# Optimization experiments

Hardware: AMD Instinct MI355X
Metric: run time of the kernel (lower is better)

The kernel has to match this reference:

```python
import jax, jax.numpy as jnp
from jax import lax
import numpy as np

A = 9                 # 3 scales x 3 ratios
PRE_NMS_TOPN = 4000
POST_NMS_TOPN = 2000
NMS_THRESH = 0.7
MIN_SIZE = 16.0       # min_size * im_scale (im_info scale = 1)
NEG_INF = -1e9


def generate_anchors(base_size=16, ratios=(0.5, 1.0, 2.0), scales=(8, 16, 32)):
    ratios = np.array(ratios, dtype=np.float64)
    scales = np.array(scales, dtype=np.float64)
    w = h = float(base_size)
    xc = yc = 0.5 * (base_size - 1)
    size = w * h
    ws_r = np.round(np.sqrt(size / ratios))          # [3]
    hs_r = np.round(ws_r * ratios)                   # [3]
    ws = (ws_r[:, None] * scales[None, :]).reshape(-1)   # [9]
    hs = (hs_r[:, None] * scales[None, :]).reshape(-1)   # [9]
    anchors = np.stack([xc - 0.5 * (ws - 1), yc - 0.5 * (hs - 1),
                        xc + 0.5 * (ws - 1), yc + 0.5 * (hs - 1)], axis=1)
    return anchors.astype(np.float32)                # [9,4]


def _conv(x, w, b, padding):
    y = lax.conv_general_dilated(x, w, (1, 1), padding,
                                 dimension_numbers=('NCHW', 'OIHW', 'NCHW'))
    return y + b[None, :, None, None]


def _bbox_transform_inv(anchors, deltas):
    w = anchors[:, 2] - anchors[:, 0] + 1.0
    h = anchors[:, 3] - anchors[:, 1] + 1.0
    cx = anchors[:, 0] + 0.5 * w
    cy = anchors[:, 1] + 0.5 * h
    pcx = deltas[:, 0] * w + cx
    pcy = deltas[:, 1] * h + cy
    pw = jnp.exp(deltas[:, 2]) * w
    ph = jnp.exp(deltas[:, 3]) * h
    return jnp.stack([pcx - 0.5 * pw, pcy - 0.5 * ph,
                      pcx + 0.5 * pw, pcy + 0.5 * ph], axis=1)


def _greedy_nms(boxes, keep_init, thresh):
    # boxes already sorted by descending score; keep_init masks invalid rows
    x1, y1, x2, y2 = boxes[:, 0], boxes[:, 1], boxes[:, 2], boxes[:, 3]
    areas = (x2 - x1 + 1.0) * (y2 - y1 + 1.0)
    xx1 = jnp.maximum(x1[:, None], x1[None, :])
    yy1 = jnp.maximum(y1[:, None], y1[None, :])
    xx2 = jnp.minimum(x2[:, None], x2[None, :])
    yy2 = jnp.minimum(y2[:, None], y2[None, :])
    inter = jnp.maximum(0.0, xx2 - xx1 + 1.0) * jnp.maximum(0.0, yy2 - yy1 + 1.0)
    iou = inter / (areas[:, None] + areas[None, :] - inter)   # [N,N]
    n = boxes.shape[0]
    idx = jnp.arange(n)

    def body(i, keep):
        suppress = keep[i] & (iou[i] > thresh) & (idx > i)
        return keep & ~suppress

    return lax.fori_loop(0, n, body, keep_init)


def reference(im, feats, w_conv, b_conv, w_cls, b_cls, w_reg, b_reg):
    im_h, im_w = im.shape[2], im.shape[3]
    fh, fw = feats.shape[2], feats.shape[3]
    stride = round(im_w / fw)

    # RPN head (classifier)
    hid = jax.nn.relu(_conv(feats, w_conv, b_conv, 'SAME'))
    rpn_map = _conv(hid, w_cls, b_cls, 'SAME')       # [1, 2A, fh, fw]
    rpn_bbox = _conv(hid, w_reg, b_reg, 'SAME')      # [1, 4A, fh, fw]

    # anchor generation: [K*A, 4], shift-major / anchor-minor
    base = jnp.asarray(generate_anchors())
    sx = jnp.arange(fw, dtype=jnp.float32) * stride
    sy = jnp.arange(fh, dtype=jnp.float32) * stride
    sxx, syy = jnp.meshgrid(sx, sy)                  # [fh, fw]
    shifts = jnp.stack([sxx.ravel(), syy.ravel(), sxx.ravel(), syy.ravel()], 1)
    anchors = (base[None, :, :] + shifts[:, None, :]).reshape(-1, 4)

    # predictions, flattened in (h, w, a) order to match anchors
    deltas = rpn_bbox.transpose(0, 2, 3, 1).reshape(-1, 4)
    scores = rpn_map[:, A:, :, :].transpose(0, 2, 3, 1).reshape(-1)

    proposals = _bbox_transform_inv(anchors, deltas)
    # clip_boxes to image
    proposals = jnp.stack([
        jnp.clip(proposals[:, 0], 0.0, im_w - 1.0),
        jnp.clip(proposals[:, 1], 0.0, im_h - 1.0),
        jnp.clip(proposals[:, 2], 0.0, im_w - 1.0),
        jnp.clip(proposals[:, 3], 0.0, im_h - 1.0)], axis=1)

    # filter_boxes (min_size) expressed as a score mask (jit-friendly)
    ws = proposals[:, 2] - proposals[:, 0] + 1.0
    hs = proposals[:, 3] - proposals[:, 1] + 1.0
    valid = (ws >= MIN_SIZE) & (hs >= MIN_SIZE)
    masked_scores = jnp.where(valid, scores, NEG_INF)

    # sort descending, take pre_nms_topN
    order = jnp.argsort(-masked_scores)[:PRE_NMS_TOPN]
    top_boxes = proposals[order]
    top_scores = masked_scores[order]
    keep_init = top_scores > NEG_INF / 2

    keep = _greedy_nms(top_boxes, keep_init, NMS_THRESH)

    # take first post_nms_topN kept (already in score order), padded with zeros
    rank = jnp.cumsum(keep) - 1
    take = keep & (rank < POST_NMS_TOPN)
    dst = jnp.where(take, rank, 0)
    out_boxes = jnp.zeros((POST_NMS_TOPN, 4), dtype=top_boxes.dtype)
    out_boxes = out_boxes.at[dst].add(jnp.where(take[:, None], top_boxes, 0.0))
    out_scores = jnp.zeros((POST_NMS_TOPN, 1), dtype=top_scores.dtype)
    out_scores = out_scores.at[dst].add(jnp.where(take[:, None], top_scores[:, None], 0.0))
    return out_boxes, out_scores


def setup_inputs() -> dict:
    key = jax.random.key(0)
    ks = jax.random.split(key, 8)
    # small weight scale keeps exp(dw) in a sane range, as a trained RPN would
    return {
        'im': jax.random.normal(ks[0], (1, 3, 800, 1216), jnp.float32),
        'feats': jax.random.normal(ks[1], (1, 1024, 50, 76), jnp.float32),
        'w_conv': jax.random.normal(ks[2], (512, 1024, 3, 3), jnp.float32) * 0.001,
        'b_conv': jnp.zeros((512,), jnp.float32),
        'w_cls': jax.random.normal(ks[3], (18, 512, 1, 1), jnp.float32) * 0.01,
        'b_cls': jnp.zeros((18,), jnp.float32),
        'w_reg': jax.random.normal(ks[4], (36, 512, 1, 1), jnp.float32) * 0.01,
        'b_reg': jnp.zeros((36,), jnp.float32),
    }
```

## Files before the change

kernel.cpp:

```cpp
#include <hip/hip_runtime.h>
#include <stdint.h>
#include <math.h>

typedef unsigned long long u64;
typedef unsigned int u32;

#define CIN     1024
#define COUT    512
#define FH      50
#define FW      76
#define QP      80
#define HIDP    4096
#define FPITCH  4160
#define NPOS    3800
#define NA      34200
#define PRE_N   4000
#define POST_N  2000
#define MASKW   63
#define TBN     4032
#define KSLICES 8
#define CPS     128
#define QT      256

#define P0 (3*CIN*FPITCH)
#define P2 (512*48)
#define P3 65536

__device__ __forceinline__ void async16(const float* g, float* l) {
  __builtin_amdgcn_global_load_lds(
      (__attribute__((address_space(1))) void*)(g),
      (__attribute__((address_space(3))) void*)(l), 16, 0, 0);
}

__global__ void k_prep(const float* __restrict__ feats,
                       const float* __restrict__ w_cls, const float* __restrict__ b_cls,
                       const float* __restrict__ w_reg, const float* __restrict__ b_reg,
                       float* __restrict__ fpad3, float* __restrict__ wT, float* __restrict__ bT,
                       u32* __restrict__ hist, u32* __restrict__ ctrl,
                       double4* __restrict__ tb, float* __restrict__ ts) {
  int idx = blockIdx.x * 256 + threadIdx.x;
  if (idx < P0) {
    int tc = idx / (CIN * FPITCH);
    int rem = idx - tc * (CIN * FPITCH);
    int cin = rem / FPITCH;
    int j = rem - cin * FPITCH + tc;
    float v = 0.f;
    if (j < FPITCH) {
      int r = j / QP, u = j - r * QP;
      if (r >= 1 && r <= FH && u >= 1 && u <= FW)
        v = feats[cin * (FH * FW) + (r - 1) * FW + (u - 1)];
    }
    fpad3[idx] = v;
    return;
  }
  idx -= P0;
  if (idx < P2) {
    int c = idx / 48, o = idx - c * 48;
    float v = 0.f;
    if (o < 9) v = w_cls[(size_t)(9 + o) * 512 + c];
    else if (o < 45) v = w_reg[(size_t)(o - 9) * 512 + c];
    wT[idx] = v;
    return;
  }
  idx -= P2;
  if (idx < P3) {
    hist[idx] = 0;
    if (idx < 8) ctrl[idx] = 0;
    if (idx < 48) bT[idx] = (idx < 9) ? b_cls[9 + idx] : (idx < 45 ? b_reg[idx - 9] : 0.f);
    if (idx >= PRE_N && idx < TBN) { tb[idx] = make_double4(0.0, 0.0, 0.0, 0.0); ts[idx] = -1.0e9f; }
  }
}

__global__ void k_wt(const float* __restrict__ w, float* __restrict__ wt) {
  __shared__ float t[64][65];
  int k0 = blockIdx.x * 64, oc0 = blockIdx.y * 64;
  int tx = threadIdx.x & 63, tg = threadIdx.x >> 6;
#pragma unroll
  for (int rr = 0; rr < 16; rr++) {
    int row = tg * 16 + rr;
    t[row][tx] = w[(size_t)(oc0 + row) * 9216 + k0 + tx];
  }
  __syncthreads();
#pragma unroll
  for (int rr = 0; rr < 16; rr++) {
    int kr = tg * 16 + rr;
    wt[(size_t)(k0 + kr) * 512 + oc0 + tx] = t[tx][kr];
  }
}

__global__ __launch_bounds__(256, 4) void k_conv(const float* __restrict__ fpad3,
                                                 const float* __restrict__ wt,
                                                 float* __restrict__ hidp) {
  __shared__ __align__(16) float Bl[3][9][QT];
  const int tid = threadIdx.x;
  const int lane = tid & 63;
  const int wv = __builtin_amdgcn_readfirstlane(tid >> 6);
  const int q0 = blockIdx.x * QT;
  const int ws = (blockIdx.y << 2) + wv;
  const int c0 = blockIdx.z * CPS;

  const int rA = wv;
  const int rB = wv + 4;
  u32 offA = (u32)(rA % 3) * (CIN * FPITCH) + (u32)(rA / 3) * QP + q0 + lane * 4;
  u32 offB = (u32)(rB % 3) * (CIN * FPITCH) + (u32)(rB / 3) * QP + q0 + lane * 4;
  u32 offC = 2u * (CIN * FPITCH) + 2u * QP + q0 + lane * 4;

  float acc32[8][4];
  double acc64[8][4];
#pragma unroll
  for (int i = 0; i < 8; i++)
#pragma unroll
    for (int j = 0; j < 4; j++) { acc32[i][j] = 0.f; acc64[i][j] = 0.0; }

#define STAGE(buf, s)  do {                                                     \
    const float* _b = fpad3 + (size_t)(c0 + (s)) * FPITCH;                      \
    async16(_b + offA, &Bl[buf][rA][0]);                                        \
    async16(_b + offB, &Bl[buf][rB][0]);                                        \
    if (wv == 0) async16(_b + offC, &Bl[buf][8][0]);                            \
  } while (0)

  STAGE(0, 0);
  STAGE(1, 1);

#pragma unroll 1
  for (int s = 0; s < CPS; s++) {
    if (s + 1 < CPS) {
      if (wv == 0) asm volatile("s_waitcnt vmcnt(3)" ::: "memory");
      else         asm volatile("s_waitcnt vmcnt(2)" ::: "memory");
    } else {
      asm volatile("s_waitcnt vmcnt(0)" ::: "memory");
    }
    __builtin_amdgcn_s_barrier();
    __builtin_amdgcn_sched_barrier(0);
    const int b0 = s % 3;
    if (s + 2 < CPS) STAGE((s + 2) % 3, s + 2);
    const float* wp = wt + ((size_t)(c0 + s) * 9 << 9) + (ws << 3);
#pragma unroll
    for (int ks = 0; ks < 9; ks++) {
      float4 b4 = *(const float4*)&Bl[b0][ks][lane * 4];
      const float* w8 = wp + (ks << 9);
#pragma unroll
      for (int i = 0; i < 8; i++) {
        float w = w8[i];
        acc32[i][0] = fmaf(w, b4.x, acc32[i][0]);
        acc32[i][1] = fmaf(w, b4.y, acc32[i][1]);
        acc32[i][2] = fmaf(w, b4.z, acc32[i][2]);
        acc32[i][3] = fmaf(w, b4.w, acc32[i][3]);
      }
    }
    if ((s & 7) == 7) {
#pragma unroll
      for (int i = 0; i < 8; i++)
#pragma unroll
        for (int j = 0; j < 4; j++) { acc64[i][j] += (double)acc32[i][j]; acc32[i][j] = 0.f; }
    }
  }
#undef STAGE

#pragma unroll
  for (int i = 0; i < 8; i++) {
    float4 o;
    o.x = (float)acc64[i][0];
    o.y = (float)acc64[i][1];
    o.z = (float)acc64[i][2];
    o.w = (float)acc64[i][3];
    *(float4*)&hidp[((size_t)(blockIdx.z * COUT + (ws << 3) + i) << 12) + q0 + lane * 4] = o;
  }
}

__global__ void k_reduce(const float* __restrict__ hidp, const float* __restrict__ bconv,
                         float* __restrict__ hid) {
  int idx = blockIdx.x * 256 + threadIdx.x;
  int oc = idx >> 12;
  double s = 0.0;
#pragma unroll
  for (int z = 0; z < KSLICES; z++)
    s += (double)hidp[idx + ((size_t)z << 21)];
  s += (double)bconv[oc];
  hid[idx] = s > 0.0 ? (float)s : 0.f;
}

__global__ __launch_bounds__(256, 8) void k_head(const float* __restrict__ hid,
                                                 const float* __restrict__ wT,
                                                 const float* __restrict__ bT,
                                                 float* __restrict__ scoresb,
                                                 float* __restrict__ deltab) {
  int lane = threadIdx.x & 63;
  int wv = threadIdx.x >> 6;
  int q = blockIdx.x * 64 + lane;
  int og = blockIdx.y * 12 + wv * 3;
  double acc0 = 0.0, acc1 = 0.0, acc2 = 0.0;
#pragma unroll 4
  for (int c = 0; c < 512; c++) {
    double hv = (double)hid[((size_t)c << 12) + q];
    const float* wr = wT + c * 48 + og;
    acc0 += hv * (double)wr[0];
    acc1 += hv * (double)wr[1];
    acc2 += hv * (double)wr[2];
  }
  int y = q / QP, x = q - y * QP;
  if (x < FW && y < FH) {
    int pos = y * FW + x;
    double a[3] = {acc0, acc1, acc2};
#pragma unroll
    for (int j = 0; j < 3; j++) {
      int o = og + j;
      float r = (float)(a[j] + (double)bT[o]);
      if (o < 9)       scoresb[o * NPOS + pos] = r;
      else if (o < 45) deltab[(o - 9) * NPOS + pos] = r;
    }
  }
}

__device__ __constant__ float AW[9] = {184.f, 368.f, 736.f, 128.f, 256.f, 512.f, 88.f, 176.f, 352.f};
__device__ __constant__ float AH[9] = {96.f, 192.f, 384.f, 128.f, 256.f, 512.f, 176.f, 352.f, 704.f};

__global__ void k_prop(const float* __restrict__ scoresb, const float* __restrict__ deltab,
                       double4* __restrict__ boxesd, u64* __restrict__ keys,
                       float* __restrict__ smask, u32* __restrict__ hist,
                       float* __restrict__ dout) {
  int g = blockIdx.x * 256 + threadIdx.x;
  if (g < 10000) dout[g] = 0.f;
  if (g >= NA) return;
  int pos = g / 9, a = g - pos * 9;
  int y = pos / FW, x = pos - y * FW;
  double w = (double)AW[a], h = (double)AH[a];
  double cx = x * 16.0 + 8.0, cy = y * 16.0 + 8.0;
  double d0 = (double)deltab[(4 * a + 0) * NPOS + pos];
  double d1 = (double)deltab[(4 * a + 1) * NPOS + pos];
  double d2 = (double)deltab[(4 * a + 2) * NPOS + pos];
  double d3 = (double)deltab[(4 * a + 3) * NPOS + pos];
  double pcx = d0 * w + cx, pcy = d1 * h + cy;
  double pw = exp(d2) * w, ph = exp(d3) * h;
  double px1 = fmin(fmax(pcx - 0.5 * pw, 0.0), 1215.0);
  double py1 = fmin(fmax(pcy - 0.5 * ph, 0.0), 799.0);
  double px2 = fmin(fmax(pcx + 0.5 * pw, 0.0), 1215.0);
  double py2 = fmin(fmax(pcy + 0.5 * ph, 0.0), 799.0);
  bool valid = (px2 - px1 + 1.0 >= 16.0) && (py2 - py1 + 1.0 >= 16.0);
  float sc = scoresb[a * NPOS + pos];
  float ms = valid ? sc : -1.0e9f;
  boxesd[g] = make_double4(px1, py1, px2, py2);
  smask[g] = ms;
  u32 u = __float_as_uint(ms);
  u = (u >> 31) ? ~u : (u | 0x80000000u);
  keys[g] = ((u64)u << 32) | (u32)(~(u32)g);
  atomicAdd(&hist[u >> 16], 1u);
}

__global__ void k_scan(const u32* __restrict__ hist, u32* __restrict__ ctrl) {
  __shared__ u32 cs[256];
  __shared__ u32 sfx[256];
  int t = threadIdx.x;
  u32 s = 0;
  for (int i = 0; i < 256; i++) s += hist[t * 256 + i];
  cs[t] = s;
  __syncthreads();
  if (t == 0) {
    u32 c = 0;
    for (int i = 255; i >= 0; i--) { sfx[i] = c; c += cs[i]; }
  }
  __syncthreads();
  u32 before = sfx[t];
  u32 c = 0;
  for (int b = 255; b >= 0; b--) {
    u32 hv = hist[t * 256 + b];
    if (before + c < PRE_N && before + c + hv >= PRE_N) {
      ctrl[0] = (u32)(t * 256 + b);
      ctrl[1] = before + c;
    }
    c += hv;
  }
}

__global__ void k_compact(const u64* __restrict__ keys, u32* __restrict__ ctrl,
                          u64* __restrict__ candK, u32* __restrict__ candG) {
  int g = blockIdx.x * 256 + threadIdx.x;
  if (g >= NA) return;
  u32 binB = ctrl[0];
  u64 k = keys[g];
  if ((u32)(k >> 48) >= binB) {
    u32 idx = atomicAdd(&ctrl[2], 1u);
    candK[idx] = k;
    candG[idx] = g;
  }
}

__global__ void k_rank(const u64* __restrict__ candK, const u32* __restrict__ candG,
                       const u32* __restrict__ ctrl, const double4* __restrict__ boxesd,
                       const float* __restrict__ smask, double4* __restrict__ tb,
                       float* __restrict__ ts) {
  __shared__ u64 kk[256];
  u32 m = ctrl[2];
  if (blockIdx.x * 256 >= m) return;
  int i = blockIdx.x * 256 + threadIdx.x;
  u64 my = (i < (int)m) ? candK[i] : 0ULL;
  u32 rank = 0;
  for (u32 base = 0; base < m; base += 256) {
    u32 j = base + threadIdx.x;
    kk[threadIdx.x] = (j < m) ? candK[j] : 0ULL;
    __syncthreads();
    u32 lim = m - base; if (lim > 256) lim = 256;
    for (u32 tt = 0; tt < lim; tt++) rank += (kk[tt] > my) ? 1u : 0u;
    __syncthreads();
  }
  if (i < (int)m && rank < PRE_N) {
    u32 g = candG[i];
    tb[rank] = boxesd[g];
    ts[rank] = smask[g];
  }
}

__global__ void k_mask(const double4* __restrict__ tb, u64* __restrict__ mask) {
  __shared__ double4 bx[64];
  int w = blockIdx.x;
  int i = blockIdx.y * 256 + threadIdx.x;
  if (threadIdx.x < 64) bx[threadIdx.x] = tb[w * 64 + threadIdx.x];
  __syncthreads();
  if (i >= PRE_N) return;
  double4 b = tb[i];
  double ai = (b.z - b.x + 1.0) * (b.w - b.y + 1.0);
  u64 word = 0;
#pragma unroll 8
  for (int j = 0; j < 64; j++) {
    int jg = w * 64 + j;
    double4 cc = bx[j];
    double xx1 = fmax(b.x, cc.x), yy1 = fmax(b.y, cc.y);
    double xx2 = fmin(b.z, cc.z), yy2 = fmin(b.w, cc.w);
    double iw = xx2 - xx1 + 1.0, ih = yy2 - yy1 + 1.0;
    iw = iw > 0.0 ? iw : 0.0; ih = ih > 0.0 ? ih : 0.0;
    double inter = iw * ih;
    double aj = (cc.z - cc.x + 1.0) * (cc.w - cc.y + 1.0);
    bool sup = (jg > i) && (inter > 0.7 * (ai + aj - inter));
    word |= sup ? (1ULL << j) : 0ULL;
  }
  mask[(size_t)i * MASKW + w] = word;
}

__global__ __launch_bounds__(64, 1) void k_nms(const u64* __restrict__ mask,
                                               const float* __restrict__ ts,
                                               const double4* __restrict__ tb,
                                               float* __restrict__ out) {
  int lane = threadIdx.x;
  u64 keep = 0;
  for (int w = 0; w < MASKW; w++) {
    float s = ts[w * 64 + lane];
    u64 b = __ballot(s > -5.0e8f);
    if (lane == w) keep = b;
  }
  for (int c = 0; c < MASKW; c++) {
    u64 cur = __shfl(keep, c);
    u64 D = mask[(size_t)(c * 64 + lane) * MASKW + c];
    for (int j = 0; j < 64; j++) {
      u64 Dj = __shfl(D, j);
      if ((cur >> j) & 1ULL) cur &= ~Dj;
    }
    if (lane == c) keep = cur;
    u64 supp = 0;
#pragma unroll 1
    for (int jb = 0; jb < 64; jb += 16) {
      u64 v[16];
#pragma unroll
      for (int u2 = 0; u2 < 16; u2++)
        v[u2] = (lane < MASKW) ? mask[(size_t)(c * 64 + jb + u2) * MASKW + lane] : 0ULL;
#pragma unroll
      for (int u2 = 0; u2 < 16; u2++)
        if ((cur >> (jb + u2)) & 1ULL) supp |= v[u2];
    }
    keep &= ~supp;
  }
  int pc = __popcll(keep);
  int pre = pc;
#pragma unroll
  for (int off = 1; off < 64; off <<= 1) {
    int v = __shfl_up(pre, off);
    if (lane >= off) pre += v;
  }
  pre -= pc;
#pragma unroll 1
  for (int j = 0; j < 64; j++) {
    if ((keep >> j) & 1ULL) {
      int r = pre + __popcll(keep & ((1ULL << j) - 1ULL));
      if (r < POST_N) {
        int i = lane * 64 + j;
        double4 b = tb[i];
        out[r * 4 + 0] = (float)b.x;
        out[r * 4 + 1] = (float)b.y;
        out[r * 4 + 2] = (float)b.z;
        out[r * 4 + 3] = (float)b.w;
        out[8000 + r] = ts[i];
      }
    }
  }
}

extern "C" void kernel_launch(void* const* d_in, const int* in_sizes, int n_in,
                              void* d_out, int out_size, void* d_ws, size_t ws_size,
                              hipStream_t stream) {
  const float* feats  = (const float*)d_in[1];
  const float* w_conv = (const float*)d_in[2];
  const float* b_conv = (const float*)d_in[3];
  const float* w_cls  = (const float*)d_in[4];
  const float* b_cls  = (const float*)d_in[5];
  const float* w_reg  = (const float*)d_in[6];
  const float* b_reg  = (const float*)d_in[7];
  float* out = (float*)d_out;

  char* p = (char*)d_ws;
  auto carve = [&p](size_t bytes) -> void* {
    void* r = (void*)p;
    p += (bytes + 255) & ~(size_t)255;
    return r;
  };
  float*   fpad3   = (float*)carve(sizeof(float) * (P0 + 512));
  float*   wt      = (float*)carve(sizeof(float) * 9216 * 512);
  float*   wT      = (float*)carve(sizeof(float) * P2);
  float*   bT      = (float*)carve(sizeof(float) * 48);
  float*   hid     = (float*)carve(sizeof(float) * COUT * HIDP);
  float*   hidp    = (float*)carve(sizeof(float) * KSLICES * COUT * HIDP);
  float*   scoresb = (float*)carve(sizeof(float) * 9 * NPOS);
  float*   deltab  = (float*)carve(sizeof(float) * 36 * NPOS);
  double4* boxesd  = (double4*)carve(sizeof(double4) * NA);
  u64*     keys    = (u64*)carve(sizeof(u64) * NA);
  float*   smask   = (float*)carve(sizeof(float) * NA);
  u32*     hist    = (u32*)carve(sizeof(u32) * 65536);
  u32*     ctrl    = (u32*)carve(256);
  u64*     candK   = (u64*)carve(sizeof(u64) * NA);
  u32*     candG   = (u32*)carve(sizeof(u32) * NA);
  double4* tb      = (double4*)carve(sizeof(double4) * TBN);
  float*   ts      = (float*)carve(sizeof(float) * TBN);
  u64*     maskb   = (u64*)carve(sizeof(u64) * (size_t)TBN * MASKW);
  (void)ws_size; (void)in_sizes; (void)n_in; (void)out_size;

  int prep_blocks = (P0 + P2 + P3) / 256;
  k_prep<<<prep_blocks, 256, 0, stream>>>(feats, w_cls, b_cls, w_reg, b_reg,
                                          fpad3, wT, bT, hist, ctrl, tb, ts);
  k_wt<<<dim3(144, 8), 256, 0, stream>>>(w_conv, wt);
  k_conv<<<dim3(16, 16, KSLICES), 256, 0, stream>>>(fpad3, wt, hidp);
  k_reduce<<<8192, 256, 0, stream>>>(hidp, b_conv, hid);
  k_head<<<dim3(64, 4), 256, 0, stream>>>(hid, wT, bT, scoresb, deltab);
  k_prop<<<134, 256, 0, stream>>>(scoresb, deltab, boxesd, keys, smask, hist, out);
  k_scan<<<1, 256, 0, stream>>>(hist, ctrl);
  k_compact<<<134, 256, 0, stream>>>(keys, ctrl, candK, candG);
  k_rank<<<134, 256, 0, stream>>>(candK, candG, ctrl, boxesd, smask, tb, ts);
  k_mask<<<dim3(MASKW, 16), 256, 0, stream>>>(tb, maskb);
  k_nms<<<1, 64, 0, stream>>>(maskb, ts, tb, out);
}
```

Before: 1.158 ms.

## Halve conv spatial tile to 128 positions and skip lower-triangle NMS mask loads

```diff
diff --git a/kernel.cpp b/kernel.cpp
--- a/kernel.cpp
+++ b/kernel.cpp
@@ -20,7 +20,7 @@
 #define TBN     4032
 #define KSLICES 8
 #define CPS     128
-#define QT      256
+#define QT      128
 
 #define P0 (3*CIN*FPITCH)
 #define P2 (512*48)
@@ -88,10 +88,10 @@
   }
 }
 
-__global__ __launch_bounds__(256, 4) void k_conv(const float* __restrict__ fpad3,
+__global__ __launch_bounds__(256, 6) void k_conv(const float* __restrict__ fpad3,
                                                  const float* __restrict__ wt,
                                                  float* __restrict__ hidp) {
-  __shared__ __align__(16) float Bl[3][9][QT];
+  __shared__ __align__(16) float Bl[3][10][QT];
   const int tid = threadIdx.x;
   const int lane = tid & 63;
   const int wv = __builtin_amdgcn_readfirstlane(tid >> 6);
@@ -99,24 +99,23 @@
   const int ws = (blockIdx.y << 2) + wv;
   const int c0 = blockIdx.z * CPS;
 
-  const int rA = wv;
-  const int rB = wv + 4;
-  u32 offA = (u32)(rA % 3) * (CIN * FPITCH) + (u32)(rA / 3) * QP + q0 + lane * 4;
-  u32 offB = (u32)(rB % 3) * (CIN * FPITCH) + (u32)(rB / 3) * QP + q0 + lane * 4;
-  u32 offC = 2u * (CIN * FPITCH) + 2u * QP + q0 + lane * 4;
-
-  float acc32[8][4];
-  double acc64[8][4];
-#pragma unroll
-  for (int i = 0; i < 8; i++)
-#pragma unroll
-    for (int j = 0; j < 4; j++) { acc32[i][j] = 0.f; acc64[i][j] = 0.0; }
+  int rA = 2 * wv + (lane >> 5);
+  int trA = rA / 3, tcA = rA - trA * 3;
+  u32 voffA = (u32)tcA * (CIN * FPITCH) + (u32)trA * QP + q0 + (lane & 31) * 4;
+  u32 voffB = 2u * (CIN * FPITCH) + 2u * QP + q0 + (lane & 31) * 4;
+
+  float acc32[8][2];
+  double acc64[8][2];
+#pragma unroll
+  for (int i = 0; i < 8; i++) {
+    acc32[i][0] = acc32[i][1] = 0.f;
+    acc64[i][0] = acc64[i][1] = 0.0;
+  }
 
 #define STAGE(buf, s)  do {                                                     \
     const float* _b = fpad3 + (size_t)(c0 + (s)) * FPITCH;                      \
-    async16(_b + offA, &Bl[buf][rA][0]);                                        \
-    async16(_b + offB, &Bl[buf][rB][0]);                                        \
-    if (wv == 0) async16(_b + offC, &Bl[buf][8][0]);                            \
+    async16(_b + voffA, &Bl[buf][2 * wv][0]);                                   \
+    if (wv == 0) async16(_b + voffB, &Bl[buf][8][0]);                           \
   } while (0)
 
   STAGE(0, 0);
@@ -125,8 +124,8 @@
 #pragma unroll 1
   for (int s = 0; s < CPS; s++) {
     if (s + 1 < CPS) {
-      if (wv == 0) asm volatile("s_waitcnt vmcnt(3)" ::: "memory");
-      else         asm volatile("s_waitcnt vmcnt(2)" ::: "memory");
+      if (wv == 0) asm volatile("s_waitcnt vmcnt(2)" ::: "memory");
+      else         asm volatile("s_waitcnt vmcnt(1)" ::: "memory");
     } else {
       asm volatile("s_waitcnt vmcnt(0)" ::: "memory");
     }
@@ -137,34 +136,31 @@
     const float* wp = wt + ((size_t)(c0 + s) * 9 << 9) + (ws << 3);
 #pragma unroll
     for (int ks = 0; ks < 9; ks++) {
-      float4 b4 = *(const float4*)&Bl[b0][ks][lane * 4];
+      float2 b2 = *(const float2*)&Bl[b0][ks][lane * 2];
       const float* w8 = wp + (ks << 9);
 #pragma unroll
       for (int i = 0; i < 8; i++) {
         float w = w8[i];
-        acc32[i][0] = fmaf(w, b4.x, acc32[i][0]);
-        acc32[i][1] = fmaf(w, b4.y, acc32[i][1]);
-        acc32[i][2] = fmaf(w, b4.z, acc32[i][2]);
-        acc32[i][3] = fmaf(w, b4.w, acc32[i][3]);
+        acc32[i][0] = fmaf(w, b2.x, acc32[i][0]);
+        acc32[i][1] = fmaf(w, b2.y, acc32[i][1]);
       }
     }
     if ((s & 7) == 7) {
 #pragma unroll
-      for (int i = 0; i < 8; i++)
-#pragma unroll
-        for (int j = 0; j < 4; j++) { acc64[i][j] += (double)acc32[i][j]; acc32[i][j] = 0.f; }
+      for (int i = 0; i < 8; i++) {
+        acc64[i][0] += (double)acc32[i][0]; acc32[i][0] = 0.f;
+        acc64[i][1] += (double)acc32[i][1]; acc32[i][1] = 0.f;
+      }
     }
   }
 #undef STAGE
 
 #pragma unroll
   for (int i = 0; i < 8; i++) {
-    float4 o;
+    float2 o;
     o.x = (float)acc64[i][0];
     o.y = (float)acc64[i][1];
-    o.z = (float)acc64[i][2];
-    o.w = (float)acc64[i][3];
-    *(float4*)&hidp[((size_t)(blockIdx.z * COUT + (ws << 3) + i) << 12) + q0 + lane * 4] = o;
+    *(float2*)&hidp[((size_t)(blockIdx.z * COUT + (ws << 3) + i) << 12) + q0 + lane * 2] = o;
   }
 }
 
@@ -361,7 +357,7 @@
       u64 v[16];
 #pragma unroll
       for (int u2 = 0; u2 < 16; u2++)
-        v[u2] = (lane < MASKW) ? mask[(size_t)(c * 64 + jb + u2) * MASKW + lane] : 0ULL;
+        v[u2] = (lane < MASKW && lane >= c) ? mask[(size_t)(c * 64 + jb + u2) * MASKW + lane] : 0ULL;
 #pragma unroll
       for (int u2 = 0; u2 < 16; u2++)
         if ((cur >> (jb + u2)) & 1ULL) supp |= v[u2];
@@ -435,7 +431,7 @@
   k_prep<<<prep_blocks, 256, 0, stream>>>(feats, w_cls, b_cls, w_reg, b_reg,
                                           fpad3, wT, bT, hist, ctrl, tb, ts);
   k_wt<<<dim3(144, 8), 256, 0, stream>>>(w_conv, wt);
-  k_conv<<<dim3(16, 16, KSLICES), 256, 0, stream>>>(fpad3, wt, hidp);
+  k_conv<<<dim3(32, 16, KSLICES), 256, 0, stream>>>(fpad3, wt, hidp);
   k_reduce<<<8192, 256, 0, stream>>>(hidp, b_conv, hid);
   k_head<<<dim3(64, 4), 256, 0, stream>>>(hid, wT, bT, scoresb, deltab);
   k_prop<<<134, 256, 0, stream>>>(scoresb, deltab, boxesd, keys, smask, hist, out);
```

After: 1.111 ms. 4.1% less time.
